# Kernel tuning notes

Measured on AMD Instinct MI355X. Metric: run time of the kernel, lower is better.

The kernel has to match this reference:

```python
import jax, jax.numpy as jnp
import numpy as np

B, NT, NZ, CIN, H, DOUT, L = 16, 128, 256, 3, 64, 128, 3
N = NT * NZ  # 32768 nodes
EPS = 1e-5


def _build_edges():
    # Toroidal grid: each node connects to 4 neighbors (wrap-around in theta and zeta).
    T, Z = np.meshgrid(np.arange(NT), np.arange(NZ), indexing='ij')
    curr = (T * NZ + Z).ravel()
    nbrs = np.stack([
        (((T + 1) % NT) * NZ + Z).ravel(),
        (((T - 1) % NT) * NZ + Z).ravel(),
        (T * NZ + (Z + 1) % NZ).ravel(),
        (T * NZ + (Z - 1) % NZ).ravel(),
    ], axis=1)
    src = np.repeat(curr, 4)
    dst = nbrs.ravel()
    return np.stack([src, dst]).astype(np.int32)  # (2, 4N)


def setup_inputs() -> dict:
    key = jax.random.key(0)
    ks = jax.random.split(key, 8)
    s = lambda k, shp, fan: jax.random.normal(k, shp, jnp.float32) / np.float32(np.sqrt(fan))
    return {
        'x': jax.random.normal(ks[0], (B, CIN, N), jnp.float32),
        'edge_index': jnp.asarray(_build_edges()),
        'embed_W': s(ks[1], (CIN, H), CIN),
        'embed_b': jnp.zeros((H,), jnp.float32),
        'mp_W1': s(ks[2], (L, 2 * H, H), 2 * H),
        'mp_b1': jnp.zeros((L, H), jnp.float32),
        'mp_g1': jnp.ones((L, H), jnp.float32),
        'mp_be1': jnp.zeros((L, H), jnp.float32),
        'mp_W2': s(ks[3], (L, H, H), H),
        'mp_b2': jnp.zeros((L, H), jnp.float32),
        'mp_g2': jnp.ones((L, H), jnp.float32),
        'mp_be2': jnp.zeros((L, H), jnp.float32),
        'head_W1': s(ks[4], (H, H), H),
        'head_b1': jnp.zeros((H,), jnp.float32),
        'head_W2': s(ks[5], (H, DOUT), H),
        'head_b2': jnp.zeros((DOUT,), jnp.float32),
    }


def _bn(y, g, b):
    # BatchNorm1d in training mode: biased batch stats over (batch*nodes).
    m = y.mean(axis=(0, 1))
    v = y.var(axis=(0, 1))
    return (y - m) * (g * jax.lax.rsqrt(v + EPS)) + b


def reference(x, edge_index, embed_W, embed_b, mp_W1, mp_b1, mp_g1, mp_be1,
              mp_W2, mp_b2, mp_g2, mp_be2, head_W1, head_b1, head_W2, head_b2):
    src, dst = edge_index[0], edge_index[1]
    # embedding: (B,3,N) -> (B,N,H)
    h = jax.nn.relu(jnp.einsum('bcn,ch->bnh', x, embed_W) + embed_b)
    deg = jnp.zeros((N,), x.dtype).at[dst].add(1.0)
    deg = jnp.clip(deg, 1.0)[None, :, None]  # (1,N,1), all 4 on this graph
    for l in range(L):
        # gather neighbor features and scatter-add to destination, mean aggregate
        agg = jnp.zeros_like(h).at[:, dst, :].add(h[:, src, :]) / deg
        comb = jnp.concatenate([h, agg], axis=-1)  # (B,N,2H)
        y = jax.nn.relu(_bn(comb @ mp_W1[l] + mp_b1[l], mp_g1[l], mp_be1[l]))
        y = jax.nn.relu(_bn(y @ mp_W2[l] + mp_b2[l], mp_g2[l], mp_be2[l]))
        h = y + h  # residual (c_in == c_out)
    pooled = h.mean(axis=1)  # AdaptiveAvgPool1d(1) over nodes
    return jax.nn.relu(pooled @ head_W1 + head_b1) @ head_W2 + head_b2
```

## Files before the change

kernel.cpp:

```cpp
#include <hip/hip_runtime.h>

typedef unsigned short u16;
typedef u16 u16x8 __attribute__((ext_vector_type(8)));
typedef short s16x8 __attribute__((ext_vector_type(8)));
typedef float f32x4 __attribute__((ext_vector_type(4)));

#define NNODES 32768
#define EPSV 1e-5f
#define INV_ROWS (1.0f / 524288.0f)

__device__ __forceinline__ float bf2f(u16 u) {
  union { unsigned int i; float f; } v; v.i = ((unsigned int)u) << 16; return v.f;
}
__device__ __forceinline__ u16 f2bf(float f) {
  union { float f; unsigned int i; } v; v.f = f;
  unsigned int r = v.i + 0x7FFFu + ((v.i >> 16) & 1u);
  return (u16)(r >> 16);
}

__global__ __launch_bounds__(256) void k_prep(
    const float* __restrict__ W1, const float* __restrict__ W2,
    u16* __restrict__ w1t, u16* __restrict__ w2t) {
  int idx = blockIdx.x * 256 + threadIdx.x;
  if (idx < 24576) {
    int l = idx >> 13, rem = idx & 8191;
    int n = rem >> 7, k = rem & 127;
    float w = W1[l * 8192 + k * 64 + n];
    if (k >= 64) w *= 0.25f;
    w1t[idx] = f2bf(w);
  } else {
    int idx2 = idx - 24576;
    if (idx2 < 12288) {
      int l = idx2 >> 12, rem = idx2 & 4095;
      int n = rem >> 6, k = rem & 63;
      w2t[idx2] = f2bf(W2[l * 4096 + k * 64 + n]);
    }
  }
}

__global__ __launch_bounds__(256) void k_embed(
    const float* __restrict__ x, const float* __restrict__ eW,
    const float* __restrict__ eb, u16* __restrict__ h) {
  int tid = threadIdx.x;
  int chunk = tid & 7;
  int r = blockIdx.x * 32 + (tid >> 3);
  int b = r >> 15;
  int n = r & 32767;
  const float* xb = x + (size_t)b * 3 * NNODES + n;
  float x0 = xb[0], x1 = xb[NNODES], x2 = xb[2 * NNODES];
  int c0 = chunk * 8;
  u16x8 ov;
#pragma unroll
  for (int j = 0; j < 8; ++j) {
    float acc = eb[c0 + j] + x0 * eW[c0 + j] + x1 * eW[64 + c0 + j] + x2 * eW[128 + c0 + j];
    ov[j] = f2bf(fmaxf(acc, 0.f));
  }
  *reinterpret_cast<u16x8*>(&h[(size_t)r * 64 + c0]) = ov;
}

__global__ __launch_bounds__(256) void k_gemm1(
    const u16* __restrict__ h, u16* __restrict__ ybuf,
    const u16* __restrict__ w1t, const float* __restrict__ b1,
    float* __restrict__ sums) {
  __shared__ __align__(16) u16 t_s[4][16 * 72];
  __shared__ float stat_s[4][128];

  int tid = threadIdx.x;
  int wv = tid >> 6, ln = tid & 63, ln15 = ln & 15, quad = ln >> 4;
  int blk = blockIdx.x;
  int xcd = blk & 7;
  int j = blk >> 3;
  int b = j >> 4;
  int t = xcd * 16 + (j & 15);
  const u16* hb = h + (((size_t)b) << 15) * 64;
  int tp = (t + 1) & 127, tm = (t + 127) & 127;

  s16x8 bfT[4][2], bfB[4][2];
#pragma unroll
  for (int c = 0; c < 4; ++c)
#pragma unroll
    for (int kk = 0; kk < 2; ++kk) {
      bfT[c][kk] = *reinterpret_cast<const s16x8*>(
          &w1t[(c * 16 + ln15) * 128 + kk * 32 + quad * 8]);
      bfB[c][kk] = *reinterpret_cast<const s16x8*>(
          &w1t[(c * 16 + ln15) * 128 + 64 + kk * 32 + quad * 8]);
    }

  float bias_c[4];
#pragma unroll
  for (int c = 0; c < 4; ++c) bias_c[c] = b1[c * 16 + ln15];

  float ls[4] = {0.f, 0.f, 0.f, 0.f}, ls2[4] = {0.f, 0.f, 0.f, 0.f};
  u16* ts = &t_s[wv][0];
  int cA = quad * 8;

#pragma unroll 1
  for (int st = 0; st < 4; ++st) {
    int z0 = st * 64 + wv * 16;
    int z = z0 + ln15;
    int zp = (z + 1) & 255, zm = (z + 255) & 255;
    size_t rS  = ((size_t)(t * 256 + z)) * 64;
    size_t rTp = ((size_t)(tp * 256 + z)) * 64;
    size_t rTm = ((size_t)(tm * 256 + z)) * 64;
    size_t rZp = ((size_t)(t * 256 + zp)) * 64;
    size_t rZm = ((size_t)(t * 256 + zm)) * 64;

    s16x8 s0  = *reinterpret_cast<const s16x8*>(&hb[rS + cA]);
    s16x8 s1  = *reinterpret_cast<const s16x8*>(&hb[rS + 32 + cA]);
    s16x8 n0a = *reinterpret_cast<const s16x8*>(&hb[rTp + cA]);
    s16x8 n0b = *reinterpret_cast<const s16x8*>(&hb[rTp + 32 + cA]);
    s16x8 n1a = *reinterpret_cast<const s16x8*>(&hb[rTm + cA]);
    s16x8 n1b = *reinterpret_cast<const s16x8*>(&hb[rTm + 32 + cA]);
    s16x8 n2a = *reinterpret_cast<const s16x8*>(&hb[rZp + cA]);
    s16x8 n2b = *reinterpret_cast<const s16x8*>(&hb[rZp + 32 + cA]);
    s16x8 n3a = *reinterpret_cast<const s16x8*>(&hb[rZm + cA]);
    s16x8 n3b = *reinterpret_cast<const s16x8*>(&hb[rZm + 32 + cA]);

    f32x4 acc[4];
#pragma unroll
    for (int c = 0; c < 4; ++c) acc[c] = (f32x4){0.f, 0.f, 0.f, 0.f};
#pragma unroll
    for (int c = 0; c < 4; ++c) {
      acc[c] = __builtin_amdgcn_mfma_f32_16x16x32_bf16(s0,  bfT[c][0], acc[c], 0, 0, 0);
      acc[c] = __builtin_amdgcn_mfma_f32_16x16x32_bf16(s1,  bfT[c][1], acc[c], 0, 0, 0);
      acc[c] = __builtin_amdgcn_mfma_f32_16x16x32_bf16(n0a, bfB[c][0], acc[c], 0, 0, 0);
      acc[c] = __builtin_amdgcn_mfma_f32_16x16x32_bf16(n0b, bfB[c][1], acc[c], 0, 0, 0);
      acc[c] = __builtin_amdgcn_mfma_f32_16x16x32_bf16(n1a, bfB[c][0], acc[c], 0, 0, 0);
      acc[c] = __builtin_amdgcn_mfma_f32_16x16x32_bf16(n1b, bfB[c][1], acc[c], 0, 0, 0);
      acc[c] = __builtin_amdgcn_mfma_f32_16x16x32_bf16(n2a, bfB[c][0], acc[c], 0, 0, 0);
      acc[c] = __builtin_amdgcn_mfma_f32_16x16x32_bf16(n2b, bfB[c][1], acc[c], 0, 0, 0);
      acc[c] = __builtin_amdgcn_mfma_f32_16x16x32_bf16(n3a, bfB[c][0], acc[c], 0, 0, 0);
      acc[c] = __builtin_amdgcn_mfma_f32_16x16x32_bf16(n3b, bfB[c][1], acc[c], 0, 0, 0);
    }

    __builtin_amdgcn_wave_barrier();
#pragma unroll
    for (int c = 0; c < 4; ++c)
#pragma unroll
      for (int rg = 0; rg < 4; ++rg) {
        float vy = acc[c][rg] + bias_c[c];
        ls[c] += vy;
        ls2[c] += vy * vy;
        ts[(quad * 4 + rg) * 72 + c * 16 + ln15] = f2bf(vy);
      }
    __builtin_amdgcn_wave_barrier();
    size_t R0 = (((size_t)b) << 15) + (size_t)t * 256 + z0;
    int lr = ln >> 2;
#pragma unroll
    for (int p = 0; p < 2; ++p) {
      int ck = (ln & 3) + p * 4;
      u16x8 v = *reinterpret_cast<const u16x8*>(&ts[lr * 72 + ck * 8]);
      *reinterpret_cast<u16x8*>(&ybuf[(R0 + lr) * 64 + ck * 8]) = v;
    }
    __builtin_amdgcn_wave_barrier();
  }

#pragma unroll
  for (int c = 0; c < 4; ++c) {
    ls[c]  += __shfl_xor(ls[c], 16, 64);  ls[c]  += __shfl_xor(ls[c], 32, 64);
    ls2[c] += __shfl_xor(ls2[c], 16, 64); ls2[c] += __shfl_xor(ls2[c], 32, 64);
  }
  if (ln < 16) {
#pragma unroll
    for (int c = 0; c < 4; ++c) {
      stat_s[wv][c * 16 + ln] = ls[c];
      stat_s[wv][64 + c * 16 + ln] = ls2[c];
    }
  }
  __syncthreads();
  if (tid < 128) {
    float s = stat_s[0][tid] + stat_s[1][tid] + stat_s[2][tid] + stat_s[3][tid];
    atomicAdd(&sums[xcd * 128 + tid], s);
  }
}

__global__ __launch_bounds__(256) void k_gemm2(
    u16* __restrict__ ybuf, const u16* __restrict__ w2t,
    const float* __restrict__ b2, const float* __restrict__ sums1,
    const float* __restrict__ g1, const float* __restrict__ be1,
    float* __restrict__ sums2) {
  __shared__ __align__(16) u16 t_s[4][16 * 72];
  __shared__ float s1_s[64], sh1_s[64];
  __shared__ float stat_s[4][128];

  int tid = threadIdx.x;
  int wv = tid >> 6, ln = tid & 63, ln15 = ln & 15, quad = ln >> 4;

  if (tid < 64) {
    float s = 0.f, s2 = 0.f;
#pragma unroll
    for (int sl = 0; sl < 8; ++sl) { s += sums1[sl * 128 + tid]; s2 += sums1[sl * 128 + 64 + tid]; }
    float m = s * INV_ROWS;
    float v = s2 * INV_ROWS - m * m;
    float sc = g1[tid] * rsqrtf(v + EPSV);
    s1_s[tid] = sc;
    sh1_s[tid] = be1[tid] - m * sc;
  }

  s16x8 bf[4][2];
#pragma unroll
  for (int c = 0; c < 4; ++c)
#pragma unroll
    for (int kk = 0; kk < 2; ++kk)
      bf[c][kk] = *reinterpret_cast<const s16x8*>(
          &w2t[(c * 16 + ln15) * 64 + kk * 32 + quad * 8]);

  float bias_c[4];
#pragma unroll
  for (int c = 0; c < 4; ++c) bias_c[c] = b2[c * 16 + ln15];

  __syncthreads();

  float sA[2][8], shA[2][8];
#pragma unroll
  for (int kk = 0; kk < 2; ++kk)
#pragma unroll
    for (int j = 0; j < 8; ++j) {
      int ch = kk * 32 + quad * 8 + j;
      sA[kk][j] = s1_s[ch];
      shA[kk][j] = sh1_s[ch];
    }

  float ls[4] = {0.f, 0.f, 0.f, 0.f}, ls2[4] = {0.f, 0.f, 0.f, 0.f};
  u16* ts = &t_s[wv][0];

#pragma unroll 1
  for (int st = 0; st < 4; ++st) {
    size_t r0 = (size_t)blockIdx.x * 256 + st * 64 + wv * 16;
    size_t row = r0 + ln15;
    u16x8 y0 = *reinterpret_cast<const u16x8*>(&ybuf[row * 64 + quad * 8]);
    u16x8 y1 = *reinterpret_cast<const u16x8*>(&ybuf[row * 64 + 32 + quad * 8]);
    s16x8 a0, a1;
#pragma unroll
    for (int j = 0; j < 8; ++j) {
      a0[j] = (short)f2bf(fmaxf(bf2f(y0[j]) * sA[0][j] + shA[0][j], 0.f));
      a1[j] = (short)f2bf(fmaxf(bf2f(y1[j]) * sA[1][j] + shA[1][j], 0.f));
    }

    f32x4 acc[4];
#pragma unroll
    for (int c = 0; c < 4; ++c) acc[c] = (f32x4){0.f, 0.f, 0.f, 0.f};
#pragma unroll
    for (int c = 0; c < 4; ++c) {
      acc[c] = __builtin_amdgcn_mfma_f32_16x16x32_bf16(a0, bf[c][0], acc[c], 0, 0, 0);
      acc[c] = __builtin_amdgcn_mfma_f32_16x16x32_bf16(a1, bf[c][1], acc[c], 0, 0, 0);
    }

    __builtin_amdgcn_wave_barrier();
#pragma unroll
    for (int c = 0; c < 4; ++c)
#pragma unroll
      for (int rg = 0; rg < 4; ++rg) {
        float vy = acc[c][rg] + bias_c[c];
        ls[c] += vy;
        ls2[c] += vy * vy;
        ts[(quad * 4 + rg) * 72 + c * 16 + ln15] = f2bf(vy);
      }
    __builtin_amdgcn_wave_barrier();
    int lr = ln >> 2;
#pragma unroll
    for (int p = 0; p < 2; ++p) {
      int ck = (ln & 3) + p * 4;
      u16x8 v = *reinterpret_cast<const u16x8*>(&ts[lr * 72 + ck * 8]);
      *reinterpret_cast<u16x8*>(&ybuf[(r0 + lr) * 64 + ck * 8]) = v;
    }
    __builtin_amdgcn_wave_barrier();
  }

#pragma unroll
  for (int c = 0; c < 4; ++c) {
    ls[c]  += __shfl_xor(ls[c], 16, 64);  ls[c]  += __shfl_xor(ls[c], 32, 64);
    ls2[c] += __shfl_xor(ls2[c], 16, 64); ls2[c] += __shfl_xor(ls2[c], 32, 64);
  }
  if (ln < 16) {
#pragma unroll
    for (int c = 0; c < 4; ++c) {
      stat_s[wv][c * 16 + ln] = ls[c];
      stat_s[wv][64 + c * 16 + ln] = ls2[c];
    }
  }
  __syncthreads();
  if (tid < 128) {
    float s = stat_s[0][tid] + stat_s[1][tid] + stat_s[2][tid] + stat_s[3][tid];
    atomicAdd(&sums2[(blockIdx.x & 7) * 128 + tid], s);
  }
}

__global__ __launch_bounds__(256) void k_resid(
    u16* __restrict__ h, const u16* __restrict__ zbuf,
    const float* __restrict__ sums2, const float* __restrict__ g2,
    const float* __restrict__ be2, float* __restrict__ pooled) {
  __shared__ float s2_s[64], sh2_s[64];
  __shared__ float red_s[32][68];
  int tid = threadIdx.x;
  if (tid < 64) {
    float s = 0.f, s2 = 0.f;
#pragma unroll
    for (int sl = 0; sl < 8; ++sl) { s += sums2[sl * 128 + tid]; s2 += sums2[sl * 128 + 64 + tid]; }
    float m = s * INV_ROWS;
    float v = s2 * INV_ROWS - m * m;
    float sc = g2[tid] * rsqrtf(v + EPSV);
    s2_s[tid] = sc;
    sh2_s[tid] = be2[tid] - m * sc;
  }
  __syncthreads();
  int ch0 = (tid & 7) * 8;
  float scl[8], shl[8];
#pragma unroll
  for (int j = 0; j < 8; ++j) { scl[j] = s2_s[ch0 + j]; shl[j] = sh2_s[ch0 + j]; }
  float p[8] = {0.f, 0.f, 0.f, 0.f, 0.f, 0.f, 0.f, 0.f};
  size_t base0 = (size_t)blockIdx.x * 16384 + tid * 8;
#pragma unroll 1
  for (int it = 0; it < 8; it += 2) {
    size_t ba = base0 + it * 2048;
    size_t bb = ba + 2048;
    u16x8 zva = *reinterpret_cast<const u16x8*>(&zbuf[ba]);
    u16x8 hva = *reinterpret_cast<const u16x8*>(&h[ba]);
    u16x8 zvb = *reinterpret_cast<const u16x8*>(&zbuf[bb]);
    u16x8 hvb = *reinterpret_cast<const u16x8*>(&h[bb]);
    u16x8 ova, ovb;
#pragma unroll
    for (int j = 0; j < 8; ++j) {
      float a = fmaxf(bf2f(zva[j]) * scl[j] + shl[j], 0.f);
      float nh = bf2f(hva[j]) + a;
      ova[j] = f2bf(nh);
      p[j] += bf2f(ova[j]);
    }
    *reinterpret_cast<u16x8*>(&h[ba]) = ova;
#pragma unroll
    for (int j = 0; j < 8; ++j) {
      float a = fmaxf(bf2f(zvb[j]) * scl[j] + shl[j], 0.f);
      float nh = bf2f(hvb[j]) + a;
      ovb[j] = f2bf(nh);
      p[j] += bf2f(ovb[j]);
    }
    *reinterpret_cast<u16x8*>(&h[bb]) = ovb;
  }
  if (pooled != nullptr) {
    int g = tid >> 3;
#pragma unroll
    for (int j = 0; j < 8; ++j) red_s[g][ch0 + j] = p[j];
    __syncthreads();
    if (tid < 64) {
      float s = 0.f;
#pragma unroll
      for (int gg = 0; gg < 32; ++gg) s += red_s[gg][tid];
      atomicAdd(&pooled[(blockIdx.x >> 7) * 64 + tid], s);
    }
  }
}

__global__ __launch_bounds__(256) void k_head(
    const float* __restrict__ pooled, const float* __restrict__ hW1,
    const float* __restrict__ hb1, const float* __restrict__ hW2,
    const float* __restrict__ hb2, float* __restrict__ out) {
  __shared__ float p_s[16 * 64];
  __shared__ float t1_s[16 * 64];
  int tid = threadIdx.x;
#pragma unroll
  for (int j = 0; j < 4; ++j)
    p_s[tid + 256 * j] = pooled[tid + 256 * j] * (1.0f / 32768.0f);
  __syncthreads();
#pragma unroll
  for (int j = 0; j < 4; ++j) {
    int idx = tid + 256 * j;
    int bb = idx >> 6, o = idx & 63;
    float acc = hb1[o];
    for (int k = 0; k < 64; ++k) acc += p_s[bb * 64 + k] * hW1[k * 64 + o];
    t1_s[idx] = fmaxf(acc, 0.f);
  }
  __syncthreads();
#pragma unroll
  for (int j = 0; j < 8; ++j) {
    int idx = tid + 256 * j;
    int bb = idx >> 7, o = idx & 127;
    float acc = hb2[o];
    for (int k = 0; k < 64; ++k) acc += t1_s[bb * 64 + k] * hW2[k * 128 + o];
    out[idx] = acc;
  }
}

extern "C" void kernel_launch(void* const* d_in, const int* in_sizes, int n_in,
                              void* d_out, int out_size, void* d_ws, size_t ws_size,
                              hipStream_t stream) {
  const float* x   = (const float*)d_in[0];
  const float* eW  = (const float*)d_in[2];
  const float* eb  = (const float*)d_in[3];
  const float* W1  = (const float*)d_in[4];
  const float* b1  = (const float*)d_in[5];
  const float* g1  = (const float*)d_in[6];
  const float* be1 = (const float*)d_in[7];
  const float* W2  = (const float*)d_in[8];
  const float* b2  = (const float*)d_in[9];
  const float* g2  = (const float*)d_in[10];
  const float* be2 = (const float*)d_in[11];
  const float* hW1 = (const float*)d_in[12];
  const float* hb1 = (const float*)d_in[13];
  const float* hW2 = (const float*)d_in[14];
  const float* hb2 = (const float*)d_in[15];
  float* out = (float*)d_out;

  char* ws = (char*)d_ws;
  u16* h    = (u16*)ws;
  u16* ybuf = (u16*)(ws + 67108864);
  float* stats  = (float*)(ws + 134217728);
  float* pooled = stats + 6144;
  u16* w1t = (u16*)(ws + 134217728 + 7168 * 4);
  u16* w2t = w1t + 24576;

  hipMemsetAsync(stats, 0, (6144 + 1024) * sizeof(float), stream);

  k_prep<<<144, 256, 0, stream>>>(W1, W2, w1t, w2t);
  k_embed<<<16384, 256, 0, stream>>>(x, eW, eb, h);
  for (int l = 0; l < 3; ++l) {
    float* sum1 = stats + l * 2048;
    float* sum2 = stats + l * 2048 + 1024;
    k_gemm1<<<2048, 256, 0, stream>>>(h, ybuf, w1t + l * 8192, b1 + l * 64, sum1);
    k_gemm2<<<2048, 256, 0, stream>>>(ybuf, w2t + l * 4096, b2 + l * 64,
                                      sum1, g1 + l * 64, be1 + l * 64, sum2);
    k_resid<<<2048, 256, 0, stream>>>(h, ybuf, sum2, g2 + l * 64, be2 + l * 64,
                                      (l == 2) ? pooled : nullptr);
  }
  k_head<<<1, 256, 0, stream>>>(pooled, hW1, hb1, hW2, hb2, out);
}
```

Measured before the change: 484.6 us.

## Stage neighbor rows in LDS for gemm1 and double-buffer ybuf loads in gemm2

```diff
diff --git a/kernel.cpp b/kernel.cpp
--- a/kernel.cpp
+++ b/kernel.cpp
@@ -58,11 +58,15 @@
   *reinterpret_cast<u16x8*>(&h[(size_t)r * 64 + c0]) = ov;
 }
 
+#define RSTR 72
 __global__ __launch_bounds__(256) void k_gemm1(
     const u16* __restrict__ h, u16* __restrict__ ybuf,
     const u16* __restrict__ w1t, const float* __restrict__ b1,
     float* __restrict__ sums) {
-  __shared__ __align__(16) u16 t_s[4][16 * 72];
+  __shared__ __align__(16) u16 s_self[130 * RSTR];
+  __shared__ __align__(16) u16 s_tp[128 * RSTR];
+  __shared__ __align__(16) u16 s_tm[128 * RSTR];
+  __shared__ __align__(16) u16 t_s[4][16 * RSTR];
   __shared__ float stat_s[4][128];
 
   int tid = threadIdx.x;
@@ -70,8 +74,11 @@
   int blk = blockIdx.x;
   int xcd = blk & 7;
   int j = blk >> 3;
-  int b = j >> 4;
-  int t = xcd * 16 + (j & 15);
+  int b = j >> 5;
+  int local = j & 31;
+  int t = xcd * 16 + (local >> 1);
+  int half = local & 1;
+  int z0 = half * 128;
   const u16* hb = h + (((size_t)b) << 15) * 64;
   int tp = (t + 1) & 127, tm = (t + 127) & 127;
 
@@ -86,35 +93,78 @@
           &w1t[(c * 16 + ln15) * 128 + 64 + kk * 32 + quad * 8]);
     }
 
+  {
+    u16x8 va[7];
+#pragma unroll
+    for (int ii = 0; ii < 7; ++ii) {
+      int i = tid + ii * 256;
+      int c = i & 7;
+      int r = (i >= 1040) ? ((i - 1040) >> 3) : (i >> 3);
+      int ring_t = (i >= 1040) ? tp : t;
+      int z = (i >= 1040) ? (z0 + r) : ((z0 + 255 + r) & 255);
+      va[ii] = *reinterpret_cast<const u16x8*>(&hb[((size_t)(ring_t * 256 + z)) * 64 + c * 8]);
+    }
+#pragma unroll
+    for (int ii = 0; ii < 7; ++ii) {
+      int i = tid + ii * 256;
+      int c = i & 7;
+      if (i < 1040) {
+        *reinterpret_cast<u16x8*>(&s_self[(i >> 3) * RSTR + c * 8]) = va[ii];
+      } else {
+        *reinterpret_cast<u16x8*>(&s_tp[((i - 1040) >> 3) * RSTR + c * 8]) = va[ii];
+      }
+    }
+    u16x8 vb[6];
+#pragma unroll
+    for (int ii = 0; ii < 6; ++ii) {
+      int i = tid + (ii + 7) * 256;
+      if (i < 3088) {
+        int c = i & 7;
+        int r = (i < 2064) ? ((i - 1040) >> 3) : ((i - 2064) >> 3);
+        int ring_t = (i < 2064) ? tp : tm;
+        vb[ii] = *reinterpret_cast<const u16x8*>(
+            &hb[((size_t)(ring_t * 256 + z0 + r)) * 64 + c * 8]);
+      }
+    }
+#pragma unroll
+    for (int ii = 0; ii < 6; ++ii) {
+      int i = tid + (ii + 7) * 256;
+      if (i < 3088) {
+        int c = i & 7;
+        if (i < 2064) {
+          *reinterpret_cast<u16x8*>(&s_tp[((i - 1040) >> 3) * RSTR + c * 8]) = vb[ii];
+        } else {
+          *reinterpret_cast<u16x8*>(&s_tm[((i - 2064) >> 3) * RSTR + c * 8]) = vb[ii];
+        }
+      }
+    }
+  }
+
   float bias_c[4];
 #pragma unroll
   for (int c = 0; c < 4; ++c) bias_c[c] = b1[c * 16 + ln15];
+
+  __syncthreads();
 
   float ls[4] = {0.f, 0.f, 0.f, 0.f}, ls2[4] = {0.f, 0.f, 0.f, 0.f};
   u16* ts = &t_s[wv][0];
   int cA = quad * 8;
 
-#pragma unroll 1
-  for (int st = 0; st < 4; ++st) {
-    int z0 = st * 64 + wv * 16;
-    int z = z0 + ln15;
-    int zp = (z + 1) & 255, zm = (z + 255) & 255;
-    size_t rS  = ((size_t)(t * 256 + z)) * 64;
-    size_t rTp = ((size_t)(tp * 256 + z)) * 64;
-    size_t rTm = ((size_t)(tm * 256 + z)) * 64;
-    size_t rZp = ((size_t)(t * 256 + zp)) * 64;
-    size_t rZm = ((size_t)(t * 256 + zm)) * 64;
-
-    s16x8 s0  = *reinterpret_cast<const s16x8*>(&hb[rS + cA]);
-    s16x8 s1  = *reinterpret_cast<const s16x8*>(&hb[rS + 32 + cA]);
-    s16x8 n0a = *reinterpret_cast<const s16x8*>(&hb[rTp + cA]);
-    s16x8 n0b = *reinterpret_cast<const s16x8*>(&hb[rTp + 32 + cA]);
-    s16x8 n1a = *reinterpret_cast<const s16x8*>(&hb[rTm + cA]);
-    s16x8 n1b = *reinterpret_cast<const s16x8*>(&hb[rTm + 32 + cA]);
-    s16x8 n2a = *reinterpret_cast<const s16x8*>(&hb[rZp + cA]);
-    s16x8 n2b = *reinterpret_cast<const s16x8*>(&hb[rZp + 32 + cA]);
-    s16x8 n3a = *reinterpret_cast<const s16x8*>(&hb[rZm + cA]);
-    s16x8 n3b = *reinterpret_cast<const s16x8*>(&hb[rZm + 32 + cA]);
+#pragma unroll
+  for (int st = 0; st < 2; ++st) {
+    int row0 = st * 64 + wv * 16;
+    int lr = row0 + ln15;
+
+    s16x8 s0  = *reinterpret_cast<const s16x8*>(&s_self[(lr + 1) * RSTR + cA]);
+    s16x8 s1  = *reinterpret_cast<const s16x8*>(&s_self[(lr + 1) * RSTR + 32 + cA]);
+    s16x8 n0a = *reinterpret_cast<const s16x8*>(&s_tp[lr * RSTR + cA]);
+    s16x8 n0b = *reinterpret_cast<const s16x8*>(&s_tp[lr * RSTR + 32 + cA]);
+    s16x8 n1a = *reinterpret_cast<const s16x8*>(&s_tm[lr * RSTR + cA]);
+    s16x8 n1b = *reinterpret_cast<const s16x8*>(&s_tm[lr * RSTR + 32 + cA]);
+    s16x8 n2a = *reinterpret_cast<const s16x8*>(&s_self[(lr + 2) * RSTR + cA]);
+    s16x8 n2b = *reinterpret_cast<const s16x8*>(&s_self[(lr + 2) * RSTR + 32 + cA]);
+    s16x8 n3a = *reinterpret_cast<const s16x8*>(&s_self[lr * RSTR + cA]);
+    s16x8 n3b = *reinterpret_cast<const s16x8*>(&s_self[lr * RSTR + 32 + cA]);
 
     f32x4 acc[4];
 #pragma unroll
@@ -141,16 +191,16 @@
         float vy = acc[c][rg] + bias_c[c];
         ls[c] += vy;
         ls2[c] += vy * vy;
-        ts[(quad * 4 + rg) * 72 + c * 16 + ln15] = f2bf(vy);
+        ts[(quad * 4 + rg) * RSTR + c * 16 + ln15] = f2bf(vy);
       }
     __builtin_amdgcn_wave_barrier();
-    size_t R0 = (((size_t)b) << 15) + (size_t)t * 256 + z0;
-    int lr = ln >> 2;
+    size_t R0 = (((size_t)b) << 15) + (size_t)t * 256 + z0 + row0;
+    int lr2 = ln >> 2;
 #pragma unroll
     for (int p = 0; p < 2; ++p) {
       int ck = (ln & 3) + p * 4;
-      u16x8 v = *reinterpret_cast<const u16x8*>(&ts[lr * 72 + ck * 8]);
-      *reinterpret_cast<u16x8*>(&ybuf[(R0 + lr) * 64 + ck * 8]) = v;
+      u16x8 v = *reinterpret_cast<const u16x8*>(&ts[lr2 * RSTR + ck * 8]);
+      *reinterpret_cast<u16x8*>(&ybuf[(R0 + lr2) * 64 + ck * 8]) = v;
     }
     __builtin_amdgcn_wave_barrier();
   }
@@ -179,7 +229,7 @@
     const float* __restrict__ b2, const float* __restrict__ sums1,
     const float* __restrict__ g1, const float* __restrict__ be1,
     float* __restrict__ sums2) {
-  __shared__ __align__(16) u16 t_s[4][16 * 72];
+  __shared__ __align__(16) u16 t_s[4][16 * RSTR];
   __shared__ float s1_s[64], sh1_s[64];
   __shared__ float stat_s[4][128];
 
@@ -224,19 +274,19 @@
   float ls[4] = {0.f, 0.f, 0.f, 0.f}, ls2[4] = {0.f, 0.f, 0.f, 0.f};
   u16* ts = &t_s[wv][0];
 
-#pragma unroll 1
-  for (int st = 0; st < 4; ++st) {
-    size_t r0 = (size_t)blockIdx.x * 256 + st * 64 + wv * 16;
-    size_t row = r0 + ln15;
-    u16x8 y0 = *reinterpret_cast<const u16x8*>(&ybuf[row * 64 + quad * 8]);
-    u16x8 y1 = *reinterpret_cast<const u16x8*>(&ybuf[row * 64 + 32 + quad * 8]);
+  auto ld2 = [&](int it, u16x8* Y) {
+    size_t row = (size_t)blockIdx.x * 256 + it * 64 + wv * 16 + ln15;
+    Y[0] = *reinterpret_cast<const u16x8*>(&ybuf[row * 64 + quad * 8]);
+    Y[1] = *reinterpret_cast<const u16x8*>(&ybuf[row * 64 + 32 + quad * 8]);
+  };
+
+  auto consume2 = [&](int it, u16x8* Y) {
     s16x8 a0, a1;
 #pragma unroll
     for (int j = 0; j < 8; ++j) {
-      a0[j] = (short)f2bf(fmaxf(bf2f(y0[j]) * sA[0][j] + shA[0][j], 0.f));
-      a1[j] = (short)f2bf(fmaxf(bf2f(y1[j]) * sA[1][j] + shA[1][j], 0.f));
-    }
-
+      a0[j] = (short)f2bf(fmaxf(bf2f(Y[0][j]) * sA[0][j] + shA[0][j], 0.f));
+      a1[j] = (short)f2bf(fmaxf(bf2f(Y[1][j]) * sA[1][j] + shA[1][j], 0.f));
+    }
     f32x4 acc[4];
 #pragma unroll
     for (int c = 0; c < 4; ++c) acc[c] = (f32x4){0.f, 0.f, 0.f, 0.f};
@@ -245,7 +295,6 @@
       acc[c] = __builtin_amdgcn_mfma_f32_16x16x32_bf16(a0, bf[c][0], acc[c], 0, 0, 0);
       acc[c] = __builtin_amdgcn_mfma_f32_16x16x32_bf16(a1, bf[c][1], acc[c], 0, 0, 0);
     }
-
     __builtin_amdgcn_wave_barrier();
 #pragma unroll
     for (int c = 0; c < 4; ++c)
@@ -254,17 +303,28 @@
         float vy = acc[c][rg] + bias_c[c];
         ls[c] += vy;
         ls2[c] += vy * vy;
-        ts[(quad * 4 + rg) * 72 + c * 16 + ln15] = f2bf(vy);
+        ts[(quad * 4 + rg) * RSTR + c * 16 + ln15] = f2bf(vy);
       }
     __builtin_amdgcn_wave_barrier();
+    size_t r0 = (size_t)blockIdx.x * 256 + it * 64 + wv * 16;
     int lr = ln >> 2;
 #pragma unroll
     for (int p = 0; p < 2; ++p) {
       int ck = (ln & 3) + p * 4;
-      u16x8 v = *reinterpret_cast<const u16x8*>(&ts[lr * 72 + ck * 8]);
+      u16x8 v = *reinterpret_cast<const u16x8*>(&ts[lr * RSTR + ck * 8]);
       *reinterpret_cast<u16x8*>(&ybuf[(r0 + lr) * 64 + ck * 8]) = v;
     }
     __builtin_amdgcn_wave_barrier();
+  };
+
+  u16x8 YA[2], YB[2];
+  ld2(0, YA);
+#pragma unroll 1
+  for (int it = 0; it < 4; it += 2) {
+    ld2(it + 1, YB);
+    consume2(it, YA);
+    if (it + 2 < 4) ld2(it + 2, YA);
+    consume2(it + 1, YB);
   }
 
 #pragma unroll
@@ -415,7 +475,7 @@
   for (int l = 0; l < 3; ++l) {
     float* sum1 = stats + l * 2048;
     float* sum2 = stats + l * 2048 + 1024;
-    k_gemm1<<<2048, 256, 0, stream>>>(h, ybuf, w1t + l * 8192, b1 + l * 64, sum1);
+    k_gemm1<<<4096, 256, 0, stream>>>(h, ybuf, w1t + l * 8192, b1 + l * 64, sum1);
     k_gemm2<<<2048, 256, 0, stream>>>(ybuf, w2t + l * 4096, b2 + l * 64,
                                       sum1, g1 + l * 64, be1 + l * 64, sum2);
     k_resid<<<2048, 256, 0, stream>>>(h, ybuf, sum2, g2 + l * 64, be2 + l * 64,
```

New measurement: 472.6 us. 2.5% less time.
